# Kernel optimization log

Hardware: AMD Instinct MI355X
Metric: run time of the kernel (lower is better)

## Reference

```python
import jax, jax.numpy as jnp
import numpy as np

B, N, D = 2, 2048, 1024
H, HD = 16, 64
BASE = 10000.0
INIT_STD = 0.02


def apply_rope(x, base=BASE):
    """Rotary embedding on the last dim; seq axis is axis 1.

    Works for q of shape (b, n, h, d) and k of shape (b, n, d).
    """
    d = x.shape[-1]
    n = x.shape[1]
    half = d // 2
    inv_freq = 1.0 / (base ** (jnp.arange(half, dtype=jnp.float32) / half))
    ang = jnp.arange(n, dtype=jnp.float32)[:, None] * inv_freq  # (n, d/2)
    extra = x.ndim - 3  # axes between seq axis and feature axis
    ang = ang.reshape((n,) + (1,) * extra + (half,))
    cos, sin = jnp.cos(ang), jnp.sin(ang)
    x1, x2 = jnp.split(x, 2, axis=-1)
    return jnp.concatenate([x1 * cos - x2 * sin, x2 * cos + x1 * sin], axis=-1)


def setup_inputs() -> dict:
    key = jax.random.key(0)
    kx, k1, k2, k3, k4 = jax.random.split(key, 5)
    x = jax.random.normal(kx, (B, N, D), dtype=jnp.float32)
    Wq = jax.random.normal(k1, (D, H * HD), dtype=jnp.float32) * INIT_STD
    Wkv = jax.random.normal(k2, (D, 2 * HD), dtype=jnp.float32) * INIT_STD
    Wkvh = jax.random.normal(k3, (D, 2 * H), dtype=jnp.float32) * INIT_STD
    Wo = jax.random.normal(k4, (H * HD, D), dtype=jnp.float32) * INIT_STD
    return {"x": x, "Wq": Wq, "Wkv": Wkv, "Wkvh": Wkvh, "Wo": Wo}


def reference(x, Wq, Wkv, Wkvh, Wo):
    b, n, d = x.shape
    q = (x @ Wq).reshape(b, n, H, HD)          # (b,n,h,hd)
    kv = x @ Wkv                                # (b,n,2*hd)
    kv_head = jax.nn.sigmoid(x @ Wkvh)          # (b,n,2*h)
    k, v = jnp.split(kv, 2, axis=-1)            # each (b,n,hd)
    k_head, v_head = jnp.split(kv_head, 2, axis=-1)  # each (b,n,h)

    # LRPE (rotary) on q and on the shared low-rank k
    q = apply_rope(q)
    k = apply_rope(k)

    # outer-product expansion: (b,n,h) x (b,n,hd) -> (b,n,h,hd)
    k = jnp.einsum('bnh,bnd->bnhd', k_head, k)
    v = jnp.einsum('bnh,bnd->bnhd', v_head, v)

    # causal softmax attention, scale = 1/sqrt(head_dim)
    scale = 1.0 / np.sqrt(HD)
    scores = jnp.einsum('bqhd,bkhd->bhqk', q, k) * scale
    mask = jnp.tril(jnp.ones((n, n), dtype=bool))
    scores = jnp.where(mask, scores, jnp.finfo(scores.dtype).min)
    p = jax.nn.softmax(scores, axis=-1)
    out = jnp.einsum('bhqk,bkhd->bqhd', p, v)   # (b,n,h,hd)

    out = out.reshape(b, n, H * HD)
    return out @ Wo
```

## Files before the change

kernel.cpp:

```cpp
#include <hip/hip_runtime.h>

typedef unsigned short u16;
typedef unsigned int u32;
typedef __attribute__((ext_vector_type(8))) short short8;
typedef __attribute__((ext_vector_type(4))) float f32x4;
typedef __attribute__((ext_vector_type(4))) u32 u32x4;
typedef __attribute__((ext_vector_type(2))) u32 u32x2;
typedef __attribute__((ext_vector_type(4))) u16 u16x4;

constexpr int B_ = 2, N_ = 2048, H_ = 16;
constexpr int ROWS = B_ * N_;
constexpr float LOG2E = 1.44269504088896f;

__device__ __forceinline__ float bf2f(u16 u){ union{u32 u; float f;} v; v.u = ((u32)u)<<16; return v.f; }
__device__ __forceinline__ u16 f2bf(float f){
  union{float f; u32 u;} v; v.f = f;
  u32 u = v.u; u += 0x7fffu + ((u>>16)&1u);
  return (u16)(u>>16);
}
__device__ __forceinline__ u32 cvtpk(float lo, float hi){
  u32 r; asm("v_cvt_pk_bf16_f32 %0, %1, %2" : "=v"(r) : "v"(lo), "v"(hi)); return r;
}

__global__ __launch_bounds__(256) void k_setup(const float* __restrict__ x, u16* __restrict__ xb,
                                               float2* __restrict__ tab,
                                               const float* __restrict__ Wq, const float* __restrict__ Wo,
                                               u16* __restrict__ WqT, u16* __restrict__ WoT,
                                               const float* __restrict__ Wkv, const float* __restrict__ Wkvh,
                                               u16* __restrict__ WkvT){
  __shared__ float T[64*65];
  int bid = blockIdx.x, tid = threadIdx.x;
  if (bid < 4096){
    int i = (bid*256 + tid)*4;
    f32x4 v = *(const f32x4*)(x + i);
    u16x4 o; o[0]=f2bf(v[0]); o[1]=f2bf(v[1]); o[2]=f2bf(v[2]); o[3]=f2bf(v[3]);
    *(u16x4*)(xb + i) = o;
    return;
  }
  if (bid < 4352){
    int idx = (bid-4096)*256 + tid;
    int i = idx & 31, n = idx >> 5;
    float ang = (float)n * exp2f(-(float)i * 0.4152410118609203f);
    tab[idx] = make_float2(cosf(ang), sinf(ang));
    return;
  }
  if (bid < 4864){
    int m = (bid - 4352) >> 8;
    const float* in = m ? Wo : Wq;
    u16* out = m ? WoT : WqT;
    int t2 = (bid - 4352) & 255;
    int n0 = (t2 & 15) << 6, k0 = (t2 >> 4) << 6;
    #pragma unroll
    for (int s=0; s<4; ++s){
      int chunk = tid + s*256, r = chunk >> 4, c4 = (chunk & 15) << 2;
      *(f32x4*)(&T[r*65 + c4]) = *(const f32x4*)(&in[(size_t)(k0 + r)*1024 + n0 + c4]);
    }
    __syncthreads();
    #pragma unroll
    for (int s=0; s<2; ++s){
      int chunk = tid + s*256, d = chunk >> 3, c8 = (chunk & 7) << 3;
      u16x4 o1, o2;
      #pragma unroll
      for (int j=0; j<4; ++j){ o1[j] = f2bf(T[(c8+j)*65 + d]); o2[j] = f2bf(T[(c8+4+j)*65 + d]); }
      *(u16x4*)(&out[(size_t)(n0 + d)*1024 + k0 + c8])     = o1;
      *(u16x4*)(&out[(size_t)(n0 + d)*1024 + k0 + c8 + 4]) = o2;
    }
    return;
  }
  {
    int idx = (bid - 4864)*256 + tid;
    int n = idx >> 10, k = idx & 1023;
    float v = 0.f;
    if (n < 128)      v = Wkv[k*128 + n];
    else if (n < 160) v = Wkvh[k*32 + (n-128)];
    WkvT[idx] = f2bf(v);
  }
}

template<int MODE>
__global__ __launch_bounds__(256) void k_gemm_mn(const u16* __restrict__ A, const u16* __restrict__ Bt,
                                                 void* __restrict__ Cv, float* __restrict__ proj,
                                                 const float2* __restrict__ tab,
                                                 int M, int N, int K){
  __shared__ u16 As[128*64];
  __shared__ u16 Bs[64*64];
  int ntile = N >> 6;
  int m0 = (blockIdx.x / ntile) << 7;
  int n0 = (blockIdx.x % ntile) << 6;
  int tid = threadIdx.x;
  int l = tid & 63, lr = l & 15, lc = l >> 4;
  int w = tid >> 6;
  int wm = w * 32;
  f32x4 acc[2][4] = {};
  for (int kt = 0; kt < K; kt += 64){
    __syncthreads();
    #pragma unroll
    for (int s = 0; s < 4; ++s){
      int chunk = tid + s*256, r = chunk >> 3, c8 = (chunk & 7) << 3;
      __builtin_amdgcn_global_load_lds(
        (const __attribute__((address_space(1))) u32*)(&A[(size_t)(m0 + r)*K + kt + c8]),
        (__attribute__((address_space(3))) u32*)(&As[r*64 + c8]), 16, 0, 0);
    }
    #pragma unroll
    for (int s = 0; s < 2; ++s){
      int chunk = tid + s*256, r = chunk >> 3, c8 = (chunk & 7) << 3;
      __builtin_amdgcn_global_load_lds(
        (const __attribute__((address_space(1))) u32*)(&Bt[(size_t)(n0 + r)*K + kt + c8]),
        (__attribute__((address_space(3))) u32*)(&Bs[r*64 + c8]), 16, 0, 0);
    }
    __syncthreads();
    short8 af[2][2], bfr[4][2];
    #pragma unroll
    for (int m=0; m<2; ++m)
      #pragma unroll
      for (int c=0; c<2; ++c)
        af[m][c] = *(const short8*)(&As[(wm + m*16 + lr)*64 + c*32 + lc*8]);
    #pragma unroll
    for (int n=0; n<4; ++n)
      #pragma unroll
      for (int c=0; c<2; ++c)
        bfr[n][c] = *(const short8*)(&Bs[(n*16 + lr)*64 + c*32 + lc*8]);
    __builtin_amdgcn_s_setprio(1);
    #pragma unroll
    for (int m=0; m<2; ++m)
      #pragma unroll
      for (int n=0; n<4; ++n)
        #pragma unroll
        for (int c=0; c<2; ++c)
          acc[m][n] = __builtin_amdgcn_mfma_f32_16x16x32_bf16(af[m][c], bfr[n][c], acc[m][n], 0,0,0);
    __builtin_amdgcn_s_setprio(0);
  }
  if constexpr (MODE == 0){
    float* C = (float*)Cv;
    #pragma unroll
    for (int m=0; m<2; ++m)
      #pragma unroll
      for (int n=0; n<4; ++n)
        #pragma unroll
        for (int r=0; r<4; ++r)
          C[(size_t)(m0 + wm + m*16 + lc*4 + r)*N + n0 + n*16 + lr] = acc[m][n][r];
  } else {
    if (n0 < 1024){
      u16* C = (u16*)Cv;
      #pragma unroll
      for (int m=0; m<2; ++m){
        int grow = m0 + wm + m*16 + lc*4;
        #pragma unroll
        for (int nf=0; nf<2; ++nf){
          int i = nf*16 + lr;
          #pragma unroll
          for (int r=0; r<4; ++r){
            float2 cs = tab[(size_t)((grow + r) & (N_-1))*32 + i];
            float x1 = acc[m][nf][r], x2 = acc[m][nf+2][r];
            C[(size_t)(grow + r)*1024 + n0 + i]      = f2bf(0.125f*(x1*cs.x - x2*cs.y));
            C[(size_t)(grow + r)*1024 + n0 + i + 32] = f2bf(0.125f*(x2*cs.x + x1*cs.y));
          }
        }
      }
    } else {
      int pc = n0 - 1024;
      #pragma unroll
      for (int m=0; m<2; ++m)
        #pragma unroll
        for (int n=0; n<4; ++n)
          #pragma unroll
          for (int r=0; r<4; ++r)
            proj[(size_t)(m0 + wm + m*16 + lc*4 + r)*192 + pc + n*16 + lr] = acc[m][n][r];
    }
  }
}

__global__ __launch_bounds__(256) void k_postproc2(const float* __restrict__ proj, const float2* __restrict__ tab,
                                                   u16* __restrict__ k_rope, float* __restrict__ k_head,
                                                   float* __restrict__ v_head, u16* __restrict__ vt){
  __shared__ u16 Tv[64*72];
  int n0 = blockIdx.x << 6;
  int b = n0 >> 11;
  int tid = threadIdx.x;
  #pragma unroll
  for (int s=0; s<4; ++s){
    int chunk = tid + s*256, r = chunk >> 4, c4 = (chunk & 15) << 2;
    f32x4 v = *(const f32x4*)(&proj[(size_t)(n0+r)*192 + 64 + c4]);
    u16x4 o; o[0]=f2bf(v[0]); o[1]=f2bf(v[1]); o[2]=f2bf(v[2]); o[3]=f2bf(v[3]);
    *(u16x4*)(&Tv[r*72 + c4]) = o;
  }
  int wv = tid>>6, t = tid&63;
  for (int rr = wv; rr < 64; rr += 4){
    int row = n0 + rr, n = row & (N_-1);
    const float* p = proj + (size_t)row*192;
    if (t < 32){
      float hv = 1.f/(1.f + __expf(-p[128 + t]));
      if (t < 16) k_head[((size_t)b*16 + t)*N_ + n] = hv * LOG2E;
      else        v_head[((size_t)b*16 + (t-16))*N_ + n] = hv;
      float2 cs = tab[n*32 + t];
      float k1 = p[t], k2 = p[32 + t];
      k_rope[(size_t)row*64 + t]      = f2bf(k1*cs.x - k2*cs.y);
      k_rope[(size_t)row*64 + 32 + t] = f2bf(k2*cs.x + k1*cs.y);
    }
  }
  __syncthreads();
  int nb = n0 & (N_-1);
  #pragma unroll
  for (int s=0; s<2; ++s){
    int chunk = tid + s*256, d = chunk>>3, c8 = (chunk&7)<<3;
    u32x4 o; u16* op = (u16*)&o;
    #pragma unroll
    for (int j=0; j<8; ++j) op[j] = Tv[(c8+j)*72 + d];
    *(u32x4*)(&vt[((size_t)b*64 + d)*N_ + nb + c8]) = o;
  }
}

__global__ __launch_bounds__(256, 4) void k_attn9(const u16* __restrict__ q_bf, const u16* __restrict__ k_rp,
                                                  const u16* __restrict__ vt, const float* __restrict__ k_hd,
                                                  const float* __restrict__ v_hd,
                                                  u16* __restrict__ o_part, float* __restrict__ l_part){
  __shared__ u16 Ks[64*72];
  __shared__ u16 Vts[64*72];
  __shared__ u16 Ps[4][16*72];
  __shared__ float g_s[128];
  int z = blockIdx.x;
  int pidx = (int)((u32)z / 3u);
  int sp = z - pidx*3;
  int qt = 31 - (pidx >> 5);
  int h = pidx & 15, b = (pidx >> 4) & 1;
  int nt = qt + 1;
  int t0 = (sp*nt)/3, t1 = ((sp+1)*nt)/3;
  int tid = threadIdx.x, w = tid>>6, l = tid&63, lr = l&15, lc = l>>4;
  if (t0 >= t1){
    u16* op = o_part + (size_t)z*4096;
    for (int i = tid; i < 512; i += 256) *(u32x4*)(op + i*8) = (u32x4){0,0,0,0};
    if (tid < 64) l_part[z*64 + tid] = 0.f;
    return;
  }
  size_t rowbase = (size_t)b*N_;
  size_t qoff = (rowbase + qt*64 + w*16 + lr)*1024 + h*64;
  short8 qf0 = *(const short8*)(&q_bf[qoff + lc*8]);
  short8 qf1 = *(const short8*)(&q_bf[qoff + 32 + lc*8]);
  const float* gkp = k_hd + ((size_t)b*16 + h)*N_;
  const float* gvp = v_hd + ((size_t)b*16 + h)*N_;
  u32x4 kr[2], vr[2]; float gr;
  auto issue = [&](int t){
    int kg0 = t << 6;
    #pragma unroll
    for (int s=0; s<2; ++s){
      int chunk = tid + s*256, r = chunk>>3, c8 = (chunk&7)<<3;
      kr[s] = *(const u32x4*)(&k_rp[(rowbase + kg0 + r)*64 + c8]);
      vr[s] = *(const u32x4*)(&vt[((size_t)b*64 + r)*N_ + kg0 + c8]);
    }
    gr = (tid < 64) ? gkp[kg0 + tid] : ((tid < 128) ? gvp[kg0 + tid - 64] : 0.f);
  };
  float lsum = 0.f;
  f32x4 o[4] = {};
  issue(t0);
  for (int t = t0; t < t1; ++t){
    int kg0 = t << 6;
    __syncthreads();
    #pragma unroll
    for (int s=0; s<2; ++s){
      int chunk = tid + s*256, r = chunk>>3, c8 = (chunk&7)<<3;
      *(u32x4*)(&Ks[r*72 + c8])  = kr[s];
      *(u32x4*)(&Vts[r*72 + c8]) = vr[s];
    }
    if (tid < 128) g_s[tid] = gr;
    if (t + 1 < t1) issue(t+1);
    __syncthreads();
    f32x4 s4[4];
    __builtin_amdgcn_s_setprio(1);
    #pragma unroll
    for (int nf=0; nf<4; ++nf){
      short8 kf0 = *(const short8*)(&Ks[(nf*16+lr)*72 + lc*8]);
      short8 kf1 = *(const short8*)(&Ks[(nf*16+lr)*72 + 32 + lc*8]);
      f32x4 zz = {};
      zz = __builtin_amdgcn_mfma_f32_16x16x32_bf16(kf0, qf0, zz, 0,0,0);
      s4[nf] = __builtin_amdgcn_mfma_f32_16x16x32_bf16(kf1, qf1, zz, 0,0,0);
    }
    __builtin_amdgcn_s_setprio(0);
    #pragma unroll
    for (int nf=0; nf<4; ++nf){
      f32x4 gkv = *(const f32x4*)(&g_s[nf*16 + lc*4]);
      #pragma unroll
      for (int r=0; r<4; ++r) s4[nf][r] *= gkv[r];
    }
    if (t == qt){
      int qg = qt*64 + w*16 + lr;
      #pragma unroll
      for (int nf=0; nf<4; ++nf)
        #pragma unroll
        for (int r=0; r<4; ++r)
          if (kg0 + nf*16 + lc*4 + r > qg) s4[nf][r] = -1e30f;
    }
    #pragma unroll
    for (int nf=0; nf<4; ++nf)
      #pragma unroll
      for (int r=0; r<4; ++r){ s4[nf][r] = exp2f(s4[nf][r]); lsum += s4[nf][r]; }
    #pragma unroll
    for (int nf=0; nf<4; ++nf){
      f32x4 gvv = *(const f32x4*)(&g_s[64 + nf*16 + lc*4]);
      u32 lo = cvtpk(s4[nf][0]*gvv[0], s4[nf][1]*gvv[1]);
      u32 hi = cvtpk(s4[nf][2]*gvv[2], s4[nf][3]*gvv[3]);
      *(u32x2*)(&Ps[w][lr*72 + nf*16 + lc*4]) = (u32x2){lo, hi};
    }
    asm volatile("s_waitcnt lgkmcnt(0)" ::: "memory");
    __builtin_amdgcn_sched_barrier(0);
    short8 pf0 = *(const short8*)(&Ps[w][lr*72 + lc*8]);
    short8 pf1 = *(const short8*)(&Ps[w][lr*72 + 32 + lc*8]);
    __builtin_amdgcn_s_setprio(1);
    #pragma unroll
    for (int nf=0; nf<4; ++nf){
      short8 vf0 = *(const short8*)(&Vts[(nf*16+lr)*72 + lc*8]);
      short8 vf1 = *(const short8*)(&Vts[(nf*16+lr)*72 + 32 + lc*8]);
      o[nf] = __builtin_amdgcn_mfma_f32_16x16x32_bf16(pf0, vf0, o[nf], 0,0,0);
      o[nf] = __builtin_amdgcn_mfma_f32_16x16x32_bf16(pf1, vf1, o[nf], 0,0,0);
    }
    __builtin_amdgcn_s_setprio(0);
  }
  lsum += __shfl_xor(lsum, 16);
  lsum += __shfl_xor(lsum, 32);
  if (lc == 0) l_part[z*64 + w*16 + lr] = lsum;
  u16* op = o_part + (size_t)z*4096;
  #pragma unroll
  for (int nf=0; nf<4; ++nf)
    #pragma unroll
    for (int r=0; r<4; ++r)
      op[(w*16 + lc*4 + r)*64 + nf*16 + lr] = f2bf(o[nf][r]);
}

__global__ __launch_bounds__(256) void k_comb(const u16* __restrict__ o_part, const float* __restrict__ l_part,
                                              u16* __restrict__ attn_o){
  int z2 = blockIdx.x;
  int qt = 31 - (z2 >> 5), h = z2 & 15, b = (z2 >> 4) & 1;
  int tid = threadIdx.x;
  int q = tid >> 2, c16 = (tid & 3) << 4;
  size_t base0 = (size_t)(3*z2)*4096 + q*64 + c16;
  float lv = l_part[(3*z2)*64 + q] + l_part[(3*z2+1)*64 + q] + l_part[(3*z2+2)*64 + q];
  float rl = __builtin_amdgcn_rcpf(lv);
  union U8 { u32x4 v; u16 s[8]; };
  U8 a0, a1, b0, b1, c0, c1, r0, r1;
  a0.v = *(const u32x4*)(o_part + base0);
  a1.v = *(const u32x4*)(o_part + base0 + 8);
  b0.v = *(const u32x4*)(o_part + base0 + 4096);
  b1.v = *(const u32x4*)(o_part + base0 + 4096 + 8);
  c0.v = *(const u32x4*)(o_part + base0 + 8192);
  c1.v = *(const u32x4*)(o_part + base0 + 8192 + 8);
  #pragma unroll
  for (int j=0; j<8; ++j){
    r0.s[j] = f2bf((bf2f(a0.s[j]) + bf2f(b0.s[j]) + bf2f(c0.s[j])) * rl);
    r1.s[j] = f2bf((bf2f(a1.s[j]) + bf2f(b1.s[j]) + bf2f(c1.s[j])) * rl);
  }
  u16* outp = attn_o + ((size_t)(b*N_ + qt*64 + q))*1024 + h*64 + c16;
  *(u32x4*)outp = r0.v;
  *(u32x4*)(outp + 8) = r1.v;
}

extern "C" void kernel_launch(void* const* d_in, const int* in_sizes, int n_in,
                              void* d_out, int out_size, void* d_ws, size_t ws_size,
                              hipStream_t stream){
  const float* x    = (const float*)d_in[0];
  const float* Wq   = (const float*)d_in[1];
  const float* Wkv  = (const float*)d_in[2];
  const float* Wkvh = (const float*)d_in[3];
  const float* Wo   = (const float*)d_in[4];
  float* out = (float*)d_out;

  char* p = (char*)d_ws;
  u16* xb      = (u16*)p;   p += (size_t)ROWS*1024*2;
  u16* WT      = (u16*)p;   p += (size_t)1216*1024*2;
  u16* WoT     = (u16*)p;   p += (size_t)1024*1024*2;
  float* proj  = (float*)p; p += (size_t)ROWS*192*4;
  u16* q_bf    = (u16*)p;   p += (size_t)ROWS*1024*2;
  u16* k_rp    = (u16*)p;   p += (size_t)ROWS*64*2;
  u16* vt      = (u16*)p;   p += (size_t)B_*64*N_*2;
  float* k_hd  = (float*)p; p += (size_t)B_*H_*N_*4;
  float* v_hd  = (float*)p; p += (size_t)B_*H_*N_*4;
  float2* tab  = (float2*)p; p += (size_t)N_*32*8;
  u16* o_part  = (u16*)p;   p += (size_t)3072*4096*2;
  float* l_part= (float*)p; p += (size_t)3072*64*4;
  u16* attn_o  = xb;

  k_setup<<<4096 + 256 + 512 + 768, 256, 0, stream>>>(x, xb, tab, Wq, Wo, WT, WoT,
                                                      Wkv, Wkvh, WT + (size_t)1024*1024);
  k_gemm_mn<1><<<(ROWS/128)*(1216/64), 256, 0, stream>>>(xb, WT, q_bf, proj, tab, ROWS, 1216, 1024);
  k_postproc2<<<ROWS/64, 256, 0, stream>>>(proj, tab, k_rp, k_hd, v_hd, vt);
  k_attn9<<<3072, 256, 0, stream>>>(q_bf, k_rp, vt, k_hd, v_hd, o_part, l_part);
  k_comb<<<1024, 256, 0, stream>>>(o_part, l_part, attn_o);
  k_gemm_mn<0><<<(ROWS/128)*(1024/64), 256, 0, stream>>>(attn_o, WoT, out, nullptr, nullptr, ROWS, 1024, 1024);
}
```

Measured before the change: 113.1 us.

## Use 128x128 GEMM tiles and double-buffer K/V tiles in attention

The projection and output GEMMs move from 128x64 to 128x128 block tiles with a 2x2 wave layout, each wave computing a 64x64 sub-tile. This halves the number of blocks and raises MFMA work per shared-memory load. The fused QKV weight is padded from 1216 to 1280 columns, with a guard on the proj writes. The attention kernel double-buffers the K, V and gate shared-memory tiles so the leading __syncthreads in each iteration can be dropped. The trade-offs are more registers and LDS per block in both kernels, fewer GEMM blocks to fill the CUs, and wasted work on the padded columns.

```diff
diff --git a/kernel.cpp b/kernel.cpp
--- a/kernel.cpp
+++ b/kernel.cpp
@@ -78,40 +78,37 @@
 }
 
 template<int MODE>
-__global__ __launch_bounds__(256) void k_gemm_mn(const u16* __restrict__ A, const u16* __restrict__ Bt,
+__global__ __launch_bounds__(256) void k_gemm128(const u16* __restrict__ A, const u16* __restrict__ Bt,
                                                  void* __restrict__ Cv, float* __restrict__ proj,
                                                  const float2* __restrict__ tab,
                                                  int M, int N, int K){
   __shared__ u16 As[128*64];
-  __shared__ u16 Bs[64*64];
-  int ntile = N >> 6;
+  __shared__ u16 Bs[128*64];
+  int ntile = N >> 7;
   int m0 = (blockIdx.x / ntile) << 7;
-  int n0 = (blockIdx.x % ntile) << 6;
+  int n0 = (blockIdx.x % ntile) << 7;
   int tid = threadIdx.x;
   int l = tid & 63, lr = l & 15, lc = l >> 4;
   int w = tid >> 6;
-  int wm = w * 32;
-  f32x4 acc[2][4] = {};
+  int wm = (w >> 1) * 64, wn = (w & 1) * 64;
+  int r_st = tid >> 3, c8_st = (tid & 7) << 3;
+  f32x4 acc[4][4] = {};
   for (int kt = 0; kt < K; kt += 64){
     __syncthreads();
     #pragma unroll
     for (int s = 0; s < 4; ++s){
-      int chunk = tid + s*256, r = chunk >> 3, c8 = (chunk & 7) << 3;
+      int r = r_st + s*32;
       __builtin_amdgcn_global_load_lds(
-        (const __attribute__((address_space(1))) u32*)(&A[(size_t)(m0 + r)*K + kt + c8]),
-        (__attribute__((address_space(3))) u32*)(&As[r*64 + c8]), 16, 0, 0);
-    }
-    #pragma unroll
-    for (int s = 0; s < 2; ++s){
-      int chunk = tid + s*256, r = chunk >> 3, c8 = (chunk & 7) << 3;
+        (const __attribute__((address_space(1))) u32*)(&A[(size_t)(m0 + r)*K + kt + c8_st]),
+        (__attribute__((address_space(3))) u32*)(&As[r*64 + c8_st]), 16, 0, 0);
       __builtin_amdgcn_global_load_lds(
-        (const __attribute__((address_space(1))) u32*)(&Bt[(size_t)(n0 + r)*K + kt + c8]),
-        (__attribute__((address_space(3))) u32*)(&Bs[r*64 + c8]), 16, 0, 0);
+        (const __attribute__((address_space(1))) u32*)(&Bt[(size_t)(n0 + r)*K + kt + c8_st]),
+        (__attribute__((address_space(3))) u32*)(&Bs[r*64 + c8_st]), 16, 0, 0);
     }
     __syncthreads();
-    short8 af[2][2], bfr[4][2];
-    #pragma unroll
-    for (int m=0; m<2; ++m)
+    short8 af[4][2], bfr[4][2];
+    #pragma unroll
+    for (int m=0; m<4; ++m)
       #pragma unroll
       for (int c=0; c<2; ++c)
         af[m][c] = *(const short8*)(&As[(wm + m*16 + lr)*64 + c*32 + lc*8]);
@@ -119,10 +116,10 @@
     for (int n=0; n<4; ++n)
       #pragma unroll
       for (int c=0; c<2; ++c)
-        bfr[n][c] = *(const short8*)(&Bs[(n*16 + lr)*64 + c*32 + lc*8]);
+        bfr[n][c] = *(const short8*)(&Bs[(wn + n*16 + lr)*64 + c*32 + lc*8]);
     __builtin_amdgcn_s_setprio(1);
     #pragma unroll
-    for (int m=0; m<2; ++m)
+    for (int m=0; m<4; ++m)
       #pragma unroll
       for (int n=0; n<4; ++n)
         #pragma unroll
@@ -133,17 +130,18 @@
   if constexpr (MODE == 0){
     float* C = (float*)Cv;
     #pragma unroll
-    for (int m=0; m<2; ++m)
+    for (int m=0; m<4; ++m)
       #pragma unroll
       for (int n=0; n<4; ++n)
         #pragma unroll
         for (int r=0; r<4; ++r)
-          C[(size_t)(m0 + wm + m*16 + lc*4 + r)*N + n0 + n*16 + lr] = acc[m][n][r];
+          C[(size_t)(m0 + wm + m*16 + lc*4 + r)*N + n0 + wn + n*16 + lr] = acc[m][n][r];
   } else {
-    if (n0 < 1024){
+    if (n0 + wn < 1024){
       u16* C = (u16*)Cv;
-      #pragma unroll
-      for (int m=0; m<2; ++m){
+      int hbase = n0 + wn;
+      #pragma unroll
+      for (int m=0; m<4; ++m){
         int grow = m0 + wm + m*16 + lc*4;
         #pragma unroll
         for (int nf=0; nf<2; ++nf){
@@ -152,20 +150,24 @@
           for (int r=0; r<4; ++r){
             float2 cs = tab[(size_t)((grow + r) & (N_-1))*32 + i];
             float x1 = acc[m][nf][r], x2 = acc[m][nf+2][r];
-            C[(size_t)(grow + r)*1024 + n0 + i]      = f2bf(0.125f*(x1*cs.x - x2*cs.y));
-            C[(size_t)(grow + r)*1024 + n0 + i + 32] = f2bf(0.125f*(x2*cs.x + x1*cs.y));
+            C[(size_t)(grow + r)*1024 + hbase + i]      = f2bf(0.125f*(x1*cs.x - x2*cs.y));
+            C[(size_t)(grow + r)*1024 + hbase + i + 32] = f2bf(0.125f*(x2*cs.x + x1*cs.y));
           }
         }
       }
     } else {
-      int pc = n0 - 1024;
-      #pragma unroll
-      for (int m=0; m<2; ++m)
-        #pragma unroll
-        for (int n=0; n<4; ++n)
-          #pragma unroll
-          for (int r=0; r<4; ++r)
-            proj[(size_t)(m0 + wm + m*16 + lc*4 + r)*192 + pc + n*16 + lr] = acc[m][n][r];
+      int pcb = n0 + wn - 1024;
+      #pragma unroll
+      for (int m=0; m<4; ++m)
+        #pragma unroll
+        for (int n=0; n<4; ++n){
+          int c = pcb + n*16 + lr;
+          if (c < 192){
+            #pragma unroll
+            for (int r=0; r<4; ++r)
+              proj[(size_t)(m0 + wm + m*16 + lc*4 + r)*192 + c] = acc[m][n][r];
+          }
+        }
     }
   }
 }
@@ -210,14 +212,14 @@
   }
 }
 
-__global__ __launch_bounds__(256, 4) void k_attn9(const u16* __restrict__ q_bf, const u16* __restrict__ k_rp,
-                                                  const u16* __restrict__ vt, const float* __restrict__ k_hd,
-                                                  const float* __restrict__ v_hd,
-                                                  u16* __restrict__ o_part, float* __restrict__ l_part){
-  __shared__ u16 Ks[64*72];
-  __shared__ u16 Vts[64*72];
+__global__ __launch_bounds__(256, 4) void k_attn10(const u16* __restrict__ q_bf, const u16* __restrict__ k_rp,
+                                                   const u16* __restrict__ vt, const float* __restrict__ k_hd,
+                                                   const float* __restrict__ v_hd,
+                                                   u16* __restrict__ o_part, float* __restrict__ l_part){
+  __shared__ u16 Ks[2][64*72];
+  __shared__ u16 Vts[2][64*72];
   __shared__ u16 Ps[4][16*72];
-  __shared__ float g_s[128];
+  __shared__ float g_s[2][128];
   int z = blockIdx.x;
   int pidx = (int)((u32)z / 3u);
   int sp = z - pidx*3;
@@ -254,22 +256,24 @@
   issue(t0);
   for (int t = t0; t < t1; ++t){
     int kg0 = t << 6;
-    __syncthreads();
+    int cur = t & 1;
+    u16* ksw = Ks[cur]; u16* vtw = Vts[cur];
     #pragma unroll
     for (int s=0; s<2; ++s){
       int chunk = tid + s*256, r = chunk>>3, c8 = (chunk&7)<<3;
-      *(u32x4*)(&Ks[r*72 + c8])  = kr[s];
-      *(u32x4*)(&Vts[r*72 + c8]) = vr[s];
-    }
-    if (tid < 128) g_s[tid] = gr;
+      *(u32x4*)(&ksw[r*72 + c8]) = kr[s];
+      *(u32x4*)(&vtw[r*72 + c8]) = vr[s];
+    }
+    if (tid < 128) g_s[cur][tid] = gr;
     if (t + 1 < t1) issue(t+1);
     __syncthreads();
+    const u16* ksb = Ks[cur]; const u16* vtb = Vts[cur]; const float* gsb = g_s[cur];
     f32x4 s4[4];
     __builtin_amdgcn_s_setprio(1);
     #pragma unroll
     for (int nf=0; nf<4; ++nf){
-      short8 kf0 = *(const short8*)(&Ks[(nf*16+lr)*72 + lc*8]);
-      short8 kf1 = *(const short8*)(&Ks[(nf*16+lr)*72 + 32 + lc*8]);
+      short8 kf0 = *(const short8*)(&ksb[(nf*16+lr)*72 + lc*8]);
+      short8 kf1 = *(const short8*)(&ksb[(nf*16+lr)*72 + 32 + lc*8]);
       f32x4 zz = {};
       zz = __builtin_amdgcn_mfma_f32_16x16x32_bf16(kf0, qf0, zz, 0,0,0);
       s4[nf] = __builtin_amdgcn_mfma_f32_16x16x32_bf16(kf1, qf1, zz, 0,0,0);
@@ -277,7 +281,7 @@
     __builtin_amdgcn_s_setprio(0);
     #pragma unroll
     for (int nf=0; nf<4; ++nf){
-      f32x4 gkv = *(const f32x4*)(&g_s[nf*16 + lc*4]);
+      f32x4 gkv = *(const f32x4*)(&gsb[nf*16 + lc*4]);
       #pragma unroll
       for (int r=0; r<4; ++r) s4[nf][r] *= gkv[r];
     }
@@ -295,7 +299,7 @@
       for (int r=0; r<4; ++r){ s4[nf][r] = exp2f(s4[nf][r]); lsum += s4[nf][r]; }
     #pragma unroll
     for (int nf=0; nf<4; ++nf){
-      f32x4 gvv = *(const f32x4*)(&g_s[64 + nf*16 + lc*4]);
+      f32x4 gvv = *(const f32x4*)(&gsb[64 + nf*16 + lc*4]);
       u32 lo = cvtpk(s4[nf][0]*gvv[0], s4[nf][1]*gvv[1]);
       u32 hi = cvtpk(s4[nf][2]*gvv[2], s4[nf][3]*gvv[3]);
       *(u32x2*)(&Ps[w][lr*72 + nf*16 + lc*4]) = (u32x2){lo, hi};
@@ -307,8 +311,8 @@
     __builtin_amdgcn_s_setprio(1);
     #pragma unroll
     for (int nf=0; nf<4; ++nf){
-      short8 vf0 = *(const short8*)(&Vts[(nf*16+lr)*72 + lc*8]);
-      short8 vf1 = *(const short8*)(&Vts[(nf*16+lr)*72 + 32 + lc*8]);
+      short8 vf0 = *(const short8*)(&vtb[(nf*16+lr)*72 + lc*8]);
+      short8 vf1 = *(const short8*)(&vtb[(nf*16+lr)*72 + 32 + lc*8]);
       o[nf] = __builtin_amdgcn_mfma_f32_16x16x32_bf16(pf0, vf0, o[nf], 0,0,0);
       o[nf] = __builtin_amdgcn_mfma_f32_16x16x32_bf16(pf1, vf1, o[nf], 0,0,0);
     }
@@ -364,7 +368,7 @@
 
   char* p = (char*)d_ws;
   u16* xb      = (u16*)p;   p += (size_t)ROWS*1024*2;
-  u16* WT      = (u16*)p;   p += (size_t)1216*1024*2;
+  u16* WT      = (u16*)p;   p += (size_t)1280*1024*2;
   u16* WoT     = (u16*)p;   p += (size_t)1024*1024*2;
   float* proj  = (float*)p; p += (size_t)ROWS*192*4;
   u16* q_bf    = (u16*)p;   p += (size_t)ROWS*1024*2;
@@ -377,11 +381,11 @@
   float* l_part= (float*)p; p += (size_t)3072*64*4;
   u16* attn_o  = xb;
 
-  k_setup<<<4096 + 256 + 512 + 768, 256, 0, stream>>>(x, xb, tab, Wq, Wo, WT, WoT,
-                                                      Wkv, Wkvh, WT + (size_t)1024*1024);
-  k_gemm_mn<1><<<(ROWS/128)*(1216/64), 256, 0, stream>>>(xb, WT, q_bf, proj, tab, ROWS, 1216, 1024);
+  k_setup<<<4096 + 256 + 512 + 1024, 256, 0, stream>>>(x, xb, tab, Wq, Wo, WT, WoT,
+                                                       Wkv, Wkvh, WT + (size_t)1024*1024);
+  k_gemm128<1><<<(ROWS/128)*(1280/128), 256, 0, stream>>>(xb, WT, q_bf, proj, tab, ROWS, 1280, 1024);
   k_postproc2<<<ROWS/64, 256, 0, stream>>>(proj, tab, k_rp, k_hd, v_hd, vt);
-  k_attn9<<<3072, 256, 0, stream>>>(q_bf, k_rp, vt, k_hd, v_hd, o_part, l_part);
+  k_attn10<<<3072, 256, 0, stream>>>(q_bf, k_rp, vt, k_hd, v_hd, o_part, l_part);
   k_comb<<<1024, 256, 0, stream>>>(o_part, l_part, attn_o);
-  k_gemm_mn<0><<<(ROWS/128)*(1024/64), 256, 0, stream>>>(attn_o, WoT, out, nullptr, nullptr, ROWS, 1024, 1024);
-}
+  k_gemm128<0><<<(ROWS/128)*(1024/128), 256, 0, stream>>>(attn_o, WoT, out, nullptr, nullptr, ROWS, 1024, 1024);
+}
```

New measurement: 132.4 us. +17.1%, slower.

## Widen attention query tile to 128 rows with 8 waves sharing K/V tiles

Applied to the files above, without the earlier changes.

The attention kernel now processes 128 query rows per block using 512 threads (8 waves) instead of 64 rows with 4 waves. Each K/V tile loaded into LDS is reused by twice as many query rows, which halves the K/V global traffic and staging work per query. The combine kernel and partial buffers are resized to match. The causal mask now runs on the last two key tiles, and the larger blocks give fewer, heavier work units, which may worsen load balance and occupancy.

```diff
diff --git a/kernel.cpp b/kernel.cpp
--- a/kernel.cpp
+++ b/kernel.cpp
@@ -7,6 +7,9 @@
 typedef __attribute__((ext_vector_type(4))) u32 u32x4;
 typedef __attribute__((ext_vector_type(2))) u32 u32x2;
 typedef __attribute__((ext_vector_type(4))) u16 u16x4;
+
+#define AS1 __attribute__((address_space(1)))
+#define AS3 __attribute__((address_space(3)))
 
 constexpr int B_ = 2, N_ = 2048, H_ = 16;
 constexpr int ROWS = B_ * N_;
@@ -98,15 +101,15 @@
     for (int s = 0; s < 4; ++s){
       int chunk = tid + s*256, r = chunk >> 3, c8 = (chunk & 7) << 3;
       __builtin_amdgcn_global_load_lds(
-        (const __attribute__((address_space(1))) u32*)(&A[(size_t)(m0 + r)*K + kt + c8]),
-        (__attribute__((address_space(3))) u32*)(&As[r*64 + c8]), 16, 0, 0);
+        (const AS1 u32*)(&A[(size_t)(m0 + r)*K + kt + c8]),
+        (AS3 u32*)(&As[r*64 + c8]), 16, 0, 0);
     }
     #pragma unroll
     for (int s = 0; s < 2; ++s){
       int chunk = tid + s*256, r = chunk >> 3, c8 = (chunk & 7) << 3;
       __builtin_amdgcn_global_load_lds(
-        (const __attribute__((address_space(1))) u32*)(&Bt[(size_t)(n0 + r)*K + kt + c8]),
-        (__attribute__((address_space(3))) u32*)(&Bs[r*64 + c8]), 16, 0, 0);
+        (const AS1 u32*)(&Bt[(size_t)(n0 + r)*K + kt + c8]),
+        (AS3 u32*)(&Bs[r*64 + c8]), 16, 0, 0);
     }
     __syncthreads();
     short8 af[2][2], bfr[4][2];
@@ -210,43 +213,41 @@
   }
 }
 
-__global__ __launch_bounds__(256, 4) void k_attn9(const u16* __restrict__ q_bf, const u16* __restrict__ k_rp,
-                                                  const u16* __restrict__ vt, const float* __restrict__ k_hd,
-                                                  const float* __restrict__ v_hd,
-                                                  u16* __restrict__ o_part, float* __restrict__ l_part){
+__global__ __launch_bounds__(512, 4) void k_attn11(const u16* __restrict__ q_bf, const u16* __restrict__ k_rp,
+                                                   const u16* __restrict__ vt, const float* __restrict__ k_hd,
+                                                   const float* __restrict__ v_hd,
+                                                   u16* __restrict__ o_part, float* __restrict__ l_part){
   __shared__ u16 Ks[64*72];
   __shared__ u16 Vts[64*72];
-  __shared__ u16 Ps[4][16*72];
+  __shared__ u16 Ps[8][16*72];
   __shared__ float g_s[128];
   int z = blockIdx.x;
   int pidx = (int)((u32)z / 3u);
   int sp = z - pidx*3;
-  int qt = 31 - (pidx >> 5);
+  int qt2 = 15 - (pidx >> 5);
   int h = pidx & 15, b = (pidx >> 4) & 1;
-  int nt = qt + 1;
+  int nt = 2*qt2 + 2;
   int t0 = (sp*nt)/3, t1 = ((sp+1)*nt)/3;
   int tid = threadIdx.x, w = tid>>6, l = tid&63, lr = l&15, lc = l>>4;
   if (t0 >= t1){
-    u16* op = o_part + (size_t)z*4096;
-    for (int i = tid; i < 512; i += 256) *(u32x4*)(op + i*8) = (u32x4){0,0,0,0};
-    if (tid < 64) l_part[z*64 + tid] = 0.f;
+    u16* op = o_part + (size_t)z*8192;
+    for (int i = tid; i < 1024; i += 512) *(u32x4*)(op + i*8) = (u32x4){0,0,0,0};
+    if (tid < 128) l_part[z*128 + tid] = 0.f;
     return;
   }
   size_t rowbase = (size_t)b*N_;
-  size_t qoff = (rowbase + qt*64 + w*16 + lr)*1024 + h*64;
+  int qg = qt2*128 + w*16 + lr;
+  size_t qoff = (rowbase + qg)*1024 + h*64;
   short8 qf0 = *(const short8*)(&q_bf[qoff + lc*8]);
   short8 qf1 = *(const short8*)(&q_bf[qoff + 32 + lc*8]);
   const float* gkp = k_hd + ((size_t)b*16 + h)*N_;
   const float* gvp = v_hd + ((size_t)b*16 + h)*N_;
-  u32x4 kr[2], vr[2]; float gr;
+  u32x4 kr, vr; float gr;
   auto issue = [&](int t){
     int kg0 = t << 6;
-    #pragma unroll
-    for (int s=0; s<2; ++s){
-      int chunk = tid + s*256, r = chunk>>3, c8 = (chunk&7)<<3;
-      kr[s] = *(const u32x4*)(&k_rp[(rowbase + kg0 + r)*64 + c8]);
-      vr[s] = *(const u32x4*)(&vt[((size_t)b*64 + r)*N_ + kg0 + c8]);
-    }
+    int r = tid >> 3, c8 = (tid & 7) << 3;
+    kr = *(const u32x4*)(&k_rp[(rowbase + kg0 + r)*64 + c8]);
+    vr = *(const u32x4*)(&vt[((size_t)b*64 + r)*N_ + kg0 + c8]);
     gr = (tid < 64) ? gkp[kg0 + tid] : ((tid < 128) ? gvp[kg0 + tid - 64] : 0.f);
   };
   float lsum = 0.f;
@@ -255,11 +256,10 @@
   for (int t = t0; t < t1; ++t){
     int kg0 = t << 6;
     __syncthreads();
-    #pragma unroll
-    for (int s=0; s<2; ++s){
-      int chunk = tid + s*256, r = chunk>>3, c8 = (chunk&7)<<3;
-      *(u32x4*)(&Ks[r*72 + c8])  = kr[s];
-      *(u32x4*)(&Vts[r*72 + c8]) = vr[s];
+    {
+      int r = tid >> 3, c8 = (tid & 7) << 3;
+      *(u32x4*)(&Ks[r*72 + c8])  = kr;
+      *(u32x4*)(&Vts[r*72 + c8]) = vr;
     }
     if (tid < 128) g_s[tid] = gr;
     if (t + 1 < t1) issue(t+1);
@@ -281,8 +281,7 @@
       #pragma unroll
       for (int r=0; r<4; ++r) s4[nf][r] *= gkv[r];
     }
-    if (t == qt){
-      int qg = qt*64 + w*16 + lr;
+    if (t >= 2*qt2){
       #pragma unroll
       for (int nf=0; nf<4; ++nf)
         #pragma unroll
@@ -316,8 +315,8 @@
   }
   lsum += __shfl_xor(lsum, 16);
   lsum += __shfl_xor(lsum, 32);
-  if (lc == 0) l_part[z*64 + w*16 + lr] = lsum;
-  u16* op = o_part + (size_t)z*4096;
+  if (lc == 0) l_part[z*128 + w*16 + lr] = lsum;
+  u16* op = o_part + (size_t)z*8192;
   #pragma unroll
   for (int nf=0; nf<4; ++nf)
     #pragma unroll
@@ -328,28 +327,31 @@
 __global__ __launch_bounds__(256) void k_comb(const u16* __restrict__ o_part, const float* __restrict__ l_part,
                                               u16* __restrict__ attn_o){
   int z2 = blockIdx.x;
-  int qt = 31 - (z2 >> 5), h = z2 & 15, b = (z2 >> 4) & 1;
+  int qt2 = 15 - (z2 >> 5), h = z2 & 15, b = (z2 >> 4) & 1;
   int tid = threadIdx.x;
-  int q = tid >> 2, c16 = (tid & 3) << 4;
-  size_t base0 = (size_t)(3*z2)*4096 + q*64 + c16;
-  float lv = l_part[(3*z2)*64 + q] + l_part[(3*z2+1)*64 + q] + l_part[(3*z2+2)*64 + q];
-  float rl = __builtin_amdgcn_rcpf(lv);
-  union U8 { u32x4 v; u16 s[8]; };
-  U8 a0, a1, b0, b1, c0, c1, r0, r1;
-  a0.v = *(const u32x4*)(o_part + base0);
-  a1.v = *(const u32x4*)(o_part + base0 + 8);
-  b0.v = *(const u32x4*)(o_part + base0 + 4096);
-  b1.v = *(const u32x4*)(o_part + base0 + 4096 + 8);
-  c0.v = *(const u32x4*)(o_part + base0 + 8192);
-  c1.v = *(const u32x4*)(o_part + base0 + 8192 + 8);
   #pragma unroll
-  for (int j=0; j<8; ++j){
-    r0.s[j] = f2bf((bf2f(a0.s[j]) + bf2f(b0.s[j]) + bf2f(c0.s[j])) * rl);
-    r1.s[j] = f2bf((bf2f(a1.s[j]) + bf2f(b1.s[j]) + bf2f(c1.s[j])) * rl);
-  }
-  u16* outp = attn_o + ((size_t)(b*N_ + qt*64 + q))*1024 + h*64 + c16;
-  *(u32x4*)outp = r0.v;
-  *(u32x4*)(outp + 8) = r1.v;
+  for (int qh = 0; qh < 2; ++qh){
+    int q = qh*64 + (tid >> 2), c16 = (tid & 3) << 4;
+    size_t base0 = (size_t)(3*z2)*8192 + q*64 + c16;
+    float lv = l_part[(3*z2)*128 + q] + l_part[(3*z2+1)*128 + q] + l_part[(3*z2+2)*128 + q];
+    float rl = __builtin_amdgcn_rcpf(lv);
+    union U8 { u32x4 v; u16 s[8]; };
+    U8 a0, a1, b0, b1, c0, c1, r0, r1;
+    a0.v = *(const u32x4*)(o_part + base0);
+    a1.v = *(const u32x4*)(o_part + base0 + 8);
+    b0.v = *(const u32x4*)(o_part + base0 + 8192);
+    b1.v = *(const u32x4*)(o_part + base0 + 8192 + 8);
+    c0.v = *(const u32x4*)(o_part + base0 + 16384);
+    c1.v = *(const u32x4*)(o_part + base0 + 16384 + 8);
+    #pragma unroll
+    for (int j=0; j<8; ++j){
+      r0.s[j] = f2bf((bf2f(a0.s[j]) + bf2f(b0.s[j]) + bf2f(c0.s[j])) * rl);
+      r1.s[j] = f2bf((bf2f(a1.s[j]) + bf2f(b1.s[j]) + bf2f(c1.s[j])) * rl);
+    }
+    u16* outp = attn_o + ((size_t)(b*N_ + qt2*128 + q))*1024 + h*64 + c16;
+    *(u32x4*)outp = r0.v;
+    *(u32x4*)(outp + 8) = r1.v;
+  }
 }
 
 extern "C" void kernel_launch(void* const* d_in, const int* in_sizes, int n_in,
@@ -373,15 +375,15 @@
   float* k_hd  = (float*)p; p += (size_t)B_*H_*N_*4;
   float* v_hd  = (float*)p; p += (size_t)B_*H_*N_*4;
   float2* tab  = (float2*)p; p += (size_t)N_*32*8;
-  u16* o_part  = (u16*)p;   p += (size_t)3072*4096*2;
-  float* l_part= (float*)p; p += (size_t)3072*64*4;
+  u16* o_part  = (u16*)p;   p += (size_t)1536*8192*2;
+  float* l_part= (float*)p; p += (size_t)1536*128*4;
   u16* attn_o  = xb;
 
   k_setup<<<4096 + 256 + 512 + 768, 256, 0, stream>>>(x, xb, tab, Wq, Wo, WT, WoT,
                                                       Wkv, Wkvh, WT + (size_t)1024*1024);
   k_gemm_mn<1><<<(ROWS/128)*(1216/64), 256, 0, stream>>>(xb, WT, q_bf, proj, tab, ROWS, 1216, 1024);
   k_postproc2<<<ROWS/64, 256, 0, stream>>>(proj, tab, k_rp, k_hd, v_hd, vt);
-  k_attn9<<<3072, 256, 0, stream>>>(q_bf, k_rp, vt, k_hd, v_hd, o_part, l_part);
-  k_comb<<<1024, 256, 0, stream>>>(o_part, l_part, attn_o);
+  k_attn11<<<1536, 512, 0, stream>>>(q_bf, k_rp, vt, k_hd, v_hd, o_part, l_part);
+  k_comb<<<512, 256, 0, stream>>>(o_part, l_part, attn_o);
   k_gemm_mn<0><<<(ROWS/128)*(1024/64), 256, 0, stream>>>(attn_o, WoT, out, nullptr, nullptr, ROWS, 1024, 1024);
 }
```

New measurement: 116.7 us. 1.03x slower.

## Pair complementary query tiles per attention block to share K/V loads

Applied to the files above, without the earlier changes.

Each attention block now handles two query tiles, p and 31-p, for the same batch and head. Each K/V/gate tile is staged into shared memory once and used for both queries, and the causal work per block becomes uniform. The grid halves, and the partial output and row-sum buffers and the combine kernel's indexing are re-laid out to match. In exchange, each block holds twice the register accumulators and has fewer blocks available to fill the GPU.

```diff
diff --git a/kernel.cpp b/kernel.cpp
--- a/kernel.cpp
+++ b/kernel.cpp
@@ -7,6 +7,9 @@
 typedef __attribute__((ext_vector_type(4))) u32 u32x4;
 typedef __attribute__((ext_vector_type(2))) u32 u32x2;
 typedef __attribute__((ext_vector_type(4))) u16 u16x4;
+
+#define AS1 __attribute__((address_space(1)))
+#define AS3 __attribute__((address_space(3)))
 
 constexpr int B_ = 2, N_ = 2048, H_ = 16;
 constexpr int ROWS = B_ * N_;
@@ -98,15 +101,15 @@
     for (int s = 0; s < 4; ++s){
       int chunk = tid + s*256, r = chunk >> 3, c8 = (chunk & 7) << 3;
       __builtin_amdgcn_global_load_lds(
-        (const __attribute__((address_space(1))) u32*)(&A[(size_t)(m0 + r)*K + kt + c8]),
-        (__attribute__((address_space(3))) u32*)(&As[r*64 + c8]), 16, 0, 0);
+        (const AS1 u32*)(&A[(size_t)(m0 + r)*K + kt + c8]),
+        (AS3 u32*)(&As[r*64 + c8]), 16, 0, 0);
     }
     #pragma unroll
     for (int s = 0; s < 2; ++s){
       int chunk = tid + s*256, r = chunk >> 3, c8 = (chunk & 7) << 3;
       __builtin_amdgcn_global_load_lds(
-        (const __attribute__((address_space(1))) u32*)(&Bt[(size_t)(n0 + r)*K + kt + c8]),
-        (__attribute__((address_space(3))) u32*)(&Bs[r*64 + c8]), 16, 0, 0);
+        (const AS1 u32*)(&Bt[(size_t)(n0 + r)*K + kt + c8]),
+        (AS3 u32*)(&Bs[r*64 + c8]), 16, 0, 0);
     }
     __syncthreads();
     short8 af[2][2], bfr[4][2];
@@ -210,10 +213,10 @@
   }
 }
 
-__global__ __launch_bounds__(256, 4) void k_attn9(const u16* __restrict__ q_bf, const u16* __restrict__ k_rp,
-                                                  const u16* __restrict__ vt, const float* __restrict__ k_hd,
-                                                  const float* __restrict__ v_hd,
-                                                  u16* __restrict__ o_part, float* __restrict__ l_part){
+__global__ __launch_bounds__(256, 4) void k_attn12(const u16* __restrict__ q_bf, const u16* __restrict__ k_rp,
+                                                   const u16* __restrict__ vt, const float* __restrict__ k_hd,
+                                                   const float* __restrict__ v_hd,
+                                                   u16* __restrict__ o_part, float* __restrict__ l_part){
   __shared__ u16 Ks[64*72];
   __shared__ u16 Vts[64*72];
   __shared__ u16 Ps[4][16*72];
@@ -221,21 +224,18 @@
   int z = blockIdx.x;
   int pidx = (int)((u32)z / 3u);
   int sp = z - pidx*3;
-  int qt = 31 - (pidx >> 5);
-  int h = pidx & 15, b = (pidx >> 4) & 1;
-  int nt = qt + 1;
+  int p = pidx & 15, h = (pidx >> 4) & 15, b = pidx >> 8;
+  int qta = p, qtb = 31 - p;
+  int nt = qtb + 1;
   int t0 = (sp*nt)/3, t1 = ((sp+1)*nt)/3;
   int tid = threadIdx.x, w = tid>>6, l = tid&63, lr = l&15, lc = l>>4;
-  if (t0 >= t1){
-    u16* op = o_part + (size_t)z*4096;
-    for (int i = tid; i < 512; i += 256) *(u32x4*)(op + i*8) = (u32x4){0,0,0,0};
-    if (tid < 64) l_part[z*64 + tid] = 0.f;
-    return;
-  }
   size_t rowbase = (size_t)b*N_;
-  size_t qoff = (rowbase + qt*64 + w*16 + lr)*1024 + h*64;
-  short8 qf0 = *(const short8*)(&q_bf[qoff + lc*8]);
-  short8 qf1 = *(const short8*)(&q_bf[qoff + 32 + lc*8]);
+  size_t qoff_a = (rowbase + qta*64 + w*16 + lr)*1024 + h*64;
+  size_t qoff_b = (rowbase + qtb*64 + w*16 + lr)*1024 + h*64;
+  short8 qa0 = *(const short8*)(&q_bf[qoff_a + lc*8]);
+  short8 qa1 = *(const short8*)(&q_bf[qoff_a + 32 + lc*8]);
+  short8 qb0 = *(const short8*)(&q_bf[qoff_b + lc*8]);
+  short8 qb1 = *(const short8*)(&q_bf[qoff_b + 32 + lc*8]);
   const float* gkp = k_hd + ((size_t)b*16 + h)*N_;
   const float* gvp = v_hd + ((size_t)b*16 + h)*N_;
   u32x4 kr[2], vr[2]; float gr;
@@ -249,21 +249,9 @@
     }
     gr = (tid < 64) ? gkp[kg0 + tid] : ((tid < 128) ? gvp[kg0 + tid - 64] : 0.f);
   };
-  float lsum = 0.f;
-  f32x4 o[4] = {};
-  issue(t0);
-  for (int t = t0; t < t1; ++t){
-    int kg0 = t << 6;
-    __syncthreads();
-    #pragma unroll
-    for (int s=0; s<2; ++s){
-      int chunk = tid + s*256, r = chunk>>3, c8 = (chunk&7)<<3;
-      *(u32x4*)(&Ks[r*72 + c8])  = kr[s];
-      *(u32x4*)(&Vts[r*72 + c8]) = vr[s];
-    }
-    if (tid < 128) g_s[tid] = gr;
-    if (t + 1 < t1) issue(t+1);
-    __syncthreads();
+  float lsa = 0.f, lsb = 0.f;
+  f32x4 oa[4] = {}, ob[4] = {};
+  auto process = [&](short8 q0, short8 q1, f32x4 (&o)[4], float& lsum, int qtt, int t, int kg0){
     f32x4 s4[4];
     __builtin_amdgcn_s_setprio(1);
     #pragma unroll
@@ -271,8 +259,8 @@
       short8 kf0 = *(const short8*)(&Ks[(nf*16+lr)*72 + lc*8]);
       short8 kf1 = *(const short8*)(&Ks[(nf*16+lr)*72 + 32 + lc*8]);
       f32x4 zz = {};
-      zz = __builtin_amdgcn_mfma_f32_16x16x32_bf16(kf0, qf0, zz, 0,0,0);
-      s4[nf] = __builtin_amdgcn_mfma_f32_16x16x32_bf16(kf1, qf1, zz, 0,0,0);
+      zz = __builtin_amdgcn_mfma_f32_16x16x32_bf16(kf0, q0, zz, 0,0,0);
+      s4[nf] = __builtin_amdgcn_mfma_f32_16x16x32_bf16(kf1, q1, zz, 0,0,0);
     }
     __builtin_amdgcn_s_setprio(0);
     #pragma unroll
@@ -281,8 +269,8 @@
       #pragma unroll
       for (int r=0; r<4; ++r) s4[nf][r] *= gkv[r];
     }
-    if (t == qt){
-      int qg = qt*64 + w*16 + lr;
+    if (t == qtt){
+      int qg = qtt*64 + w*16 + lr;
       #pragma unroll
       for (int nf=0; nf<4; ++nf)
         #pragma unroll
@@ -313,35 +301,60 @@
       o[nf] = __builtin_amdgcn_mfma_f32_16x16x32_bf16(pf1, vf1, o[nf], 0,0,0);
     }
     __builtin_amdgcn_s_setprio(0);
-  }
-  lsum += __shfl_xor(lsum, 16);
-  lsum += __shfl_xor(lsum, 32);
-  if (lc == 0) l_part[z*64 + w*16 + lr] = lsum;
-  u16* op = o_part + (size_t)z*4096;
+  };
+  issue(t0);
+  for (int t = t0; t < t1; ++t){
+    int kg0 = t << 6;
+    __syncthreads();
+    #pragma unroll
+    for (int s=0; s<2; ++s){
+      int chunk = tid + s*256, r = chunk>>3, c8 = (chunk&7)<<3;
+      *(u32x4*)(&Ks[r*72 + c8])  = kr[s];
+      *(u32x4*)(&Vts[r*72 + c8]) = vr[s];
+    }
+    if (tid < 128) g_s[tid] = gr;
+    if (t + 1 < t1) issue(t+1);
+    __syncthreads();
+    process(qb0, qb1, ob, lsb, qtb, t, kg0);
+    if (t <= qta) process(qa0, qa1, oa, lsa, qta, t, kg0);
+  }
+  lsa += __shfl_xor(lsa, 16); lsa += __shfl_xor(lsa, 32);
+  lsb += __shfl_xor(lsb, 16); lsb += __shfl_xor(lsb, 32);
+  if (lc == 0){
+    l_part[z*128 + w*16 + lr]      = lsa;
+    l_part[z*128 + 64 + w*16 + lr] = lsb;
+  }
+  u16* op = o_part + (size_t)z*8192;
   #pragma unroll
   for (int nf=0; nf<4; ++nf)
     #pragma unroll
-    for (int r=0; r<4; ++r)
-      op[(w*16 + lc*4 + r)*64 + nf*16 + lr] = f2bf(o[nf][r]);
+    for (int r=0; r<4; ++r){
+      op[(w*16 + lc*4 + r)*64 + nf*16 + lr]        = f2bf(oa[nf][r]);
+      op[4096 + (w*16 + lc*4 + r)*64 + nf*16 + lr] = f2bf(ob[nf][r]);
+    }
 }
 
 __global__ __launch_bounds__(256) void k_comb(const u16* __restrict__ o_part, const float* __restrict__ l_part,
                                               u16* __restrict__ attn_o){
   int z2 = blockIdx.x;
-  int qt = 31 - (z2 >> 5), h = z2 & 15, b = (z2 >> 4) & 1;
+  int h = z2 & 15, b = (z2 >> 4) & 1, qt = z2 >> 5;
+  int p  = (qt < 16) ? qt : 31 - qt;
+  int hs = (qt < 16) ? 0 : 1;
+  int pidx = (b << 8) | (h << 4) | p;
+  size_t zb = (size_t)3*pidx;
   int tid = threadIdx.x;
   int q = tid >> 2, c16 = (tid & 3) << 4;
-  size_t base0 = (size_t)(3*z2)*4096 + q*64 + c16;
-  float lv = l_part[(3*z2)*64 + q] + l_part[(3*z2+1)*64 + q] + l_part[(3*z2+2)*64 + q];
+  size_t base0 = zb*8192 + (size_t)hs*4096 + q*64 + c16;
+  float lv = l_part[zb*128 + hs*64 + q] + l_part[(zb+1)*128 + hs*64 + q] + l_part[(zb+2)*128 + hs*64 + q];
   float rl = __builtin_amdgcn_rcpf(lv);
   union U8 { u32x4 v; u16 s[8]; };
   U8 a0, a1, b0, b1, c0, c1, r0, r1;
   a0.v = *(const u32x4*)(o_part + base0);
   a1.v = *(const u32x4*)(o_part + base0 + 8);
-  b0.v = *(const u32x4*)(o_part + base0 + 4096);
-  b1.v = *(const u32x4*)(o_part + base0 + 4096 + 8);
-  c0.v = *(const u32x4*)(o_part + base0 + 8192);
-  c1.v = *(const u32x4*)(o_part + base0 + 8192 + 8);
+  b0.v = *(const u32x4*)(o_part + base0 + 8192);
+  b1.v = *(const u32x4*)(o_part + base0 + 8192 + 8);
+  c0.v = *(const u32x4*)(o_part + base0 + 16384);
+  c1.v = *(const u32x4*)(o_part + base0 + 16384 + 8);
   #pragma unroll
   for (int j=0; j<8; ++j){
     r0.s[j] = f2bf((bf2f(a0.s[j]) + bf2f(b0.s[j]) + bf2f(c0.s[j])) * rl);
@@ -373,15 +386,15 @@
   float* k_hd  = (float*)p; p += (size_t)B_*H_*N_*4;
   float* v_hd  = (float*)p; p += (size_t)B_*H_*N_*4;
   float2* tab  = (float2*)p; p += (size_t)N_*32*8;
-  u16* o_part  = (u16*)p;   p += (size_t)3072*4096*2;
-  float* l_part= (float*)p; p += (size_t)3072*64*4;
+  u16* o_part  = (u16*)p;   p += (size_t)1536*8192*2;
+  float* l_part= (float*)p; p += (size_t)1536*128*4;
   u16* attn_o  = xb;
 
   k_setup<<<4096 + 256 + 512 + 768, 256, 0, stream>>>(x, xb, tab, Wq, Wo, WT, WoT,
                                                       Wkv, Wkvh, WT + (size_t)1024*1024);
   k_gemm_mn<1><<<(ROWS/128)*(1216/64), 256, 0, stream>>>(xb, WT, q_bf, proj, tab, ROWS, 1216, 1024);
   k_postproc2<<<ROWS/64, 256, 0, stream>>>(proj, tab, k_rp, k_hd, v_hd, vt);
-  k_attn9<<<3072, 256, 0, stream>>>(q_bf, k_rp, vt, k_hd, v_hd, o_part, l_part);
+  k_attn12<<<1536, 256, 0, stream>>>(q_bf, k_rp, vt, k_hd, v_hd, o_part, l_part);
   k_comb<<<1024, 256, 0, stream>>>(o_part, l_part, attn_o);
   k_gemm_mn<0><<<(ROWS/128)*(1024/64), 256, 0, stream>>>(attn_o, WoT, out, nullptr, nullptr, ROWS, 1024, 1024);
 }
```

New measurement: 133.5 us. +18.1%, slower.
